# Kernel optimization log

Measured on AMD Instinct MI355X. Metric: run time of the kernel, lower is better.

## Reference

```python
import jax, jax.numpy as jnp
import numpy as np

D_H = 768
HEAD = 12
D_ATTN = D_H // HEAD


def setup_inputs() -> dict:
    key = jax.random.key(0)
    ks = jax.random.split(key, 9)
    bz, slen = 2, 4096
    scale = 1.0 / np.sqrt(D_H)
    return {
        "v": jax.random.normal(ks[0], (bz, slen, D_H), jnp.float32),
        "k": jax.random.normal(ks[1], (bz, slen, D_H), jnp.float32),
        "q": jax.random.normal(ks[2], (bz, slen, D_H), jnp.float32),
        "mask": jax.random.randint(ks[3], (bz, 1, 1, slen), 0, 2, jnp.int32),
        "w_v": jax.random.normal(ks[4], (D_H, D_H), jnp.float32) * scale,
        "w_k": jax.random.normal(ks[5], (D_H, D_H), jnp.float32) * scale,
        "w_q": jax.random.normal(ks[6], (D_H, D_H), jnp.float32) * scale,
        "w_o": jax.random.normal(ks[7], (D_H, D_H), jnp.float32) * scale,
        "b_o": jax.random.normal(ks[8], (D_H,), jnp.float32) * 0.02,
    }


def _split_head(x, seq_len):
    # (bz, len, d_h) -> (bz, head, len, d_attn)
    bz = x.shape[0]
    return x.reshape(bz, seq_len, HEAD, D_ATTN).transpose(0, 2, 1, 3)


def reference(v, k, q, mask, w_v, w_k, w_q, w_o, b_o):
    len_k, len_q = k.shape[1], q.shape[1]
    vh = _split_head(v @ w_v, len_k)   # (bz, head, len_k, d_attn)
    kh = _split_head(k @ w_k, len_k)
    qh = _split_head(q @ w_q, len_q)
    # scaled dot-product attention with additive mask
    weight = jnp.einsum("bhqd,bhkd->bhqk", qh, kh) / jnp.sqrt(
        jnp.asarray(D_ATTN, jnp.float32)
    )
    weight = weight + mask.astype(weight.dtype) * (-1e9)
    scale_weight = jax.nn.softmax(weight, axis=-1)
    attn = jnp.einsum("bhqk,bhkd->bhqd", scale_weight, vh)
    attn = attn.transpose(0, 2, 1, 3).reshape(-1, len_q, D_H)
    return attn @ w_o + b_o
```

## Files before the change

kernel.cpp:

```cpp
#include <hip/hip_runtime.h>
#include <hip/hip_bf16.h>

#define SLEN 4096
#define DH 768
#define NHEAD 12
#define DA 64

using short8 = __attribute__((ext_vector_type(8))) short;
using f32x4  = __attribute__((ext_vector_type(4))) float;
typedef unsigned uv2 __attribute__((ext_vector_type(2)));

static __device__ __forceinline__ unsigned short f2b(float f) {
    union { __hip_bfloat16 h; unsigned short u; } c;
    c.h = __float2bfloat16(f);
    return c.u;
}

static __device__ __forceinline__ unsigned pkbf(float a, float b) {
    __hip_bfloat162 h = __float22bfloat162_rn(float2{a, b});
    union { __hip_bfloat162 h; unsigned u; } c; c.h = h; return c.u;
}

static __device__ __forceinline__ float fexp2(float x) {
    float r; asm("v_exp_f32 %0, %1" : "=v"(r) : "v"(x)); return r;
}

static __device__ __forceinline__ void swap32(unsigned& a, unsigned& b, int g1) {
#if __has_builtin(__builtin_amdgcn_permlane32_swap)
    uv2 r = __builtin_amdgcn_permlane32_swap(a, b, false, false);
    a = r.x; b = r.y;
#else
    unsigned own = g1 ? b : a, send = g1 ? a : b;
    unsigned recv = __shfl_xor(send, 32);
    unsigned nlo = g1 ? recv : own;
    unsigned nhi = g1 ? own : recv;
    a = nlo; b = nhi;
#endif
}

static __device__ __forceinline__ void swap16(unsigned& a, unsigned& b, int g0) {
#if __has_builtin(__builtin_amdgcn_permlane16_swap)
    uv2 r = __builtin_amdgcn_permlane16_swap(a, b, false, false);
    a = r.x; b = r.y;
#else
    unsigned own = g0 ? b : a, send = g0 ? a : b;
    unsigned recv = __shfl_xor(send, 16);
    unsigned nlo = g0 ? recv : own;
    unsigned nhi = g0 ? own : recv;
    a = nlo; b = nhi;
#endif
}

#define GLD_LDS16(gp, lp) __builtin_amdgcn_global_load_lds( \
    (const __attribute__((address_space(1))) unsigned int*)(gp), \
    (__attribute__((address_space(3))) unsigned int*)(lp), 16, 0, 0)

#define CSCALE 0.18033688011f
#define BIASSTRIDE 4352

__global__ __launch_bounds__(256) void wtrans4(const float* __restrict__ w_v, const float* __restrict__ w_k,
                                               const float* __restrict__ w_q, const float* __restrict__ w_o,
                                               unsigned short* __restrict__ WtV, unsigned short* __restrict__ WtK,
                                               unsigned short* __restrict__ WtQ, unsigned short* __restrict__ WtO,
                                               const int* __restrict__ mask, int* __restrict__ idx,
                                               float* __restrict__ biasC, int* __restrict__ nktArr) {
    const int z = blockIdx.y;
    const int t = threadIdx.x;
    if (z == 4) {
        if (blockIdx.x >= 2) return;
        __shared__ int psum[256];
        const int b = blockIdx.x;
        const int s0 = t * 16;
        const int* mb = mask + b * SLEN;
        int keep[16]; int cnt = 0;
#pragma unroll
        for (int j = 0; j < 16; ++j) { keep[j] = (mb[s0 + j] == 0); cnt += keep[j]; }
        psum[t] = cnt;
        __syncthreads();
        for (int off = 1; off < 256; off <<= 1) {
            int v = psum[t];
            int u = (t >= off) ? psum[t - off] : 0;
            __syncthreads();
            psum[t] = v + u;
            __syncthreads();
        }
        int excl = psum[t] - cnt;
        int total = psum[255];
        int* ib = idx + b * SLEN;
#pragma unroll
        for (int j = 0; j < 16; ++j)
            if (keep[j]) ib[excl++] = s0 + j;
        for (int j = total + t; j < SLEN; j += 256) ib[j] = 0;
        int nkt = (total + 63) >> 6;
        if (nkt < 2) nkt = 2;
        if (t == 0) nktArr[b] = nkt;
        float* bb = biasC + b * BIASSTRIDE;
        for (int j = t; j < BIASSTRIDE; j += 256) bb[j] = (j < total) ? 0.f : -1.442695041e9f;
        return;
    }
    const float* W = (z == 0) ? w_v : (z == 1) ? w_k : (z == 2) ? w_q : w_o;
    unsigned short* Wt = (z == 0) ? WtV : (z == 1) ? WtK : (z == 2) ? WtQ : WtO;
    __shared__ float tile[64][65];
    const int tk = blockIdx.x / 12, tn = blockIdx.x % 12;
    const int k0 = tk * 64, n0 = tn * 64;
#pragma unroll
    for (int i = 0; i < 4; ++i) {
        int uid = t + 256 * i;
        int r = uid >> 4, c = (uid & 15) * 4;
        float4 v4 = *reinterpret_cast<const float4*>(W + (size_t)(k0 + r) * DH + n0 + c);
        tile[r][c] = v4.x; tile[r][c + 1] = v4.y; tile[r][c + 2] = v4.z; tile[r][c + 3] = v4.w;
    }
    __syncthreads();
#pragma unroll
    for (int i = 0; i < 2; ++i) {
        int uid = t + 256 * i;
        int n = uid >> 3, c = (uid & 7) * 8;
        union { unsigned short us[8]; uint4 u; } pk;
#pragma unroll
        for (int j = 0; j < 8; ++j) pk.us[j] = f2b(tile[c + j][n]);
        *reinterpret_cast<uint4*>(Wt + (size_t)(n0 + n) * DH + k0 + c) = pk.u;
    }
}

__global__ __launch_bounds__(256, 3) void proj3(const float* __restrict__ vin, const float* __restrict__ kin,
                                                const float* __restrict__ qin,
                                                const unsigned short* __restrict__ WtV,
                                                const unsigned short* __restrict__ WtK,
                                                const unsigned short* __restrict__ WtQ,
                                                unsigned short* __restrict__ Vh,
                                                unsigned short* __restrict__ Kh,
                                                unsigned short* __restrict__ Qh) {
    __shared__ __align__(16) char smem[49152];
    const int t = threadIdx.x;
    const int w = t >> 6, lane = t & 63, lr = lane & 15, lg = lane >> 4;
    const int zz = blockIdx.y;
    const int z = zz / 6, panel = zz % 6;
    const float* X = (z == 0) ? vin : (z == 1) ? kin : qin;
    const unsigned short* Wt = (z == 0) ? WtV : (z == 1) ? WtK : WtQ;
    const int row0 = blockIdx.x * 128;
    const int n0 = panel * 128;

    const float* ap[4];
#pragma unroll
    for (int g = 0; g < 4; ++g) {
        int row = w * 32 + g * 8 + (lane >> 3);
        int cj = (lane & 7) ^ (row & 7);
        ap[g] = X + (size_t)(row0 + row) * DH + cj * 4;
    }
    const unsigned short* bp2[2];
#pragma unroll
    for (int g = 0; g < 2; ++g) {
        int n = w * 32 + g * 16 + (lane >> 2);
        int cj = (lane & 3) ^ (n & 3);
        bp2[g] = Wt + (size_t)(n0 + n) * DH + cj * 8;
    }

    const int arow = w * 32 + lr;
    const int lr7 = lr & 7, lr3 = lr & 3;

    f32x4 acc[2][8] = {};

#define STAGE(PAR) do {                                                              \
        char* ab_ = smem + (PAR) * 16384 + w * 4096;                                 \
        char* bb_ = smem + 32768 + (PAR) * 8192 + w * 2048;                          \
        GLD_LDS16(ap[0], ab_);         GLD_LDS16(ap[1], ab_ + 1024);                 \
        GLD_LDS16(ap[2], ab_ + 2048);  GLD_LDS16(ap[3], ab_ + 3072);                 \
        GLD_LDS16(bp2[0], bb_);        GLD_LDS16(bp2[1], bb_ + 1024);                \
        ap[0] += 32; ap[1] += 32; ap[2] += 32; ap[3] += 32;                          \
        bp2[0] += 32; bp2[1] += 32;                                                  \
    } while (0)

    STAGE(0);
    __syncthreads();

    for (int kt = 0; kt < 24; ++kt) {
        const int par = kt & 1;
        if (kt < 23) STAGE(par ^ 1);
        const char* bufA = smem + par * 16384;
        const char* bufB = smem + 32768 + par * 8192;
        short8 af[2];
#pragma unroll
        for (int mi = 0; mi < 2; ++mi) {
            int r = arow + mi * 16;
            f32x4 alo = *reinterpret_cast<const f32x4*>(bufA + r * 128 + ((2 * lg) ^ lr7) * 16);
            f32x4 ahi = *reinterpret_cast<const f32x4*>(bufA + r * 128 + ((2 * lg + 1) ^ lr7) * 16);
            union { unsigned u[4]; short8 s; } pk;
            pk.u[0] = pkbf(alo[0], alo[1]);
            pk.u[1] = pkbf(alo[2], alo[3]);
            pk.u[2] = pkbf(ahi[0], ahi[1]);
            pk.u[3] = pkbf(ahi[2], ahi[3]);
            af[mi] = pk.s;
        }
        __builtin_amdgcn_s_setprio(1);
#pragma unroll
        for (int ni = 0; ni < 8; ++ni) {
            int n = ni * 16 + lr;
            short8 bf = *reinterpret_cast<const short8*>(bufB + n * 64 + (lg ^ lr3) * 16);
            acc[0][ni] = __builtin_amdgcn_mfma_f32_16x16x32_bf16(af[0], bf, acc[0][ni], 0, 0, 0);
            acc[1][ni] = __builtin_amdgcn_mfma_f32_16x16x32_bf16(af[1], bf, acc[1][ni], 0, 0, 0);
        }
        __builtin_amdgcn_s_setprio(0);
        __syncthreads();
    }
#undef STAGE

    const int b = row0 >> 12, s0 = row0 & 4095;
    unsigned short* Y = (z == 0) ? Vh : (z == 1) ? Kh : Qh;
    const float scale = (z == 2) ? CSCALE : 1.0f;
#pragma unroll
    for (int mi = 0; mi < 2; ++mi)
#pragma unroll
        for (int ni = 0; ni < 8; ++ni) {
            int n = n0 + ni * 16 + lr;
            int h = n >> 6, d = n & 63;
#pragma unroll
            for (int r = 0; r < 4; ++r) {
                int s = s0 + w * 32 + mi * 16 + lg * 4 + r;
                Y[(size_t)((b * NHEAD + h) * SLEN + s) * DA + d] = f2b(acc[mi][ni][r] * scale);
            }
        }
}

__global__ __launch_bounds__(256) void kvcompact(const unsigned short* __restrict__ Kh,
                                                 const unsigned short* __restrict__ Vh,
                                                 unsigned short* __restrict__ Khc,
                                                 unsigned short* __restrict__ VhTc,
                                                 const int* __restrict__ idx,
                                                 const int* __restrict__ nktArr) {
    const int jt = blockIdx.x;
    const int bh = blockIdx.y;
    const int b = bh / NHEAD;
    if (jt >= nktArr[b]) return;
    const int j0 = jt * 64;
    __shared__ unsigned short tile[64][72];
    const int t = threadIdx.x;
    const int r = t >> 2, c = t & 3;
    const int src = idx[b * SLEN + j0 + r];
    const size_t kin  = ((size_t)bh * SLEN + src) * DA + c * 16;
    const size_t kout = ((size_t)bh * SLEN + j0 + r) * DA + c * 16;
    uint4 kv0 = *reinterpret_cast<const uint4*>(Kh + kin);
    uint4 kv1 = *reinterpret_cast<const uint4*>(Kh + kin + 8);
    *reinterpret_cast<uint4*>(Khc + kout) = kv0;
    *reinterpret_cast<uint4*>(Khc + kout + 8) = kv1;
    uint4 vv0 = *reinterpret_cast<const uint4*>(Vh + kin);
    uint4 vv1 = *reinterpret_cast<const uint4*>(Vh + kin + 8);
    *reinterpret_cast<uint4*>(&tile[r][c * 16]) = vv0;
    *reinterpret_cast<uint4*>(&tile[r][c * 16 + 8]) = vv1;
    __syncthreads();
    const int d = t & 63, jc = (t >> 6) * 16;
    union { unsigned short us[8]; uint4 u; } p0, p1;
#pragma unroll
    for (int j = 0; j < 8; ++j) { p0.us[j] = tile[jc + j][d]; p1.us[j] = tile[jc + 8 + j][d]; }
    unsigned short* dst = VhTc + ((size_t)bh * DA + d) * SLEN + j0 + jc;
    *reinterpret_cast<uint4*>(dst) = p0.u;
    *reinterpret_cast<uint4*>(dst + 8) = p1.u;
}

__global__ __launch_bounds__(256, 3) void attn_kernel(const unsigned short* __restrict__ Qh,
                                                      const unsigned short* __restrict__ Kh,
                                                      const unsigned short* __restrict__ VhT,
                                                      const float* __restrict__ biasC,
                                                      const int* __restrict__ nktArr,
                                                      unsigned short* __restrict__ AT) {
    __shared__ __align__(16) char smem[49152];
    const int t = threadIdx.x;
    const int w = t >> 6, lane = t & 63, lr = lane & 15, lg = lane >> 4;
    const int g0 = (lane >> 4) & 1, g1 = (lane >> 5) & 1;
    const int lr7 = lr & 7;

    const int i = blockIdx.x;
    const int bh = (i & 7) * 3 + ((i >> 3) >> 5);
    const int qb = (i >> 3) & 31;
    const int b = bh / NHEAD;
    const int q0 = qb * 128;
    const size_t base = (size_t)bh * SLEN * DA;
    const int wq0 = q0 + w * 32;
    const int nkt = nktArr[b];

    short8 qf[2][2];
#pragma unroll
    for (int mi = 0; mi < 2; ++mi)
#pragma unroll
        for (int ks = 0; ks < 2; ++ks)
            qf[mi][ks] = *reinterpret_cast<const short8*>(
                Qh + base + (size_t)(wq0 + mi * 16 + lr) * DA + ks * 32 + lg * 8);

    const int uid0 = (w << 6) | lane;
    const int r0 = uid0 >> 3;
    const int sc0 = ((uid0 & 7) ^ (r0 & 7)) * 8;
    const unsigned short* kp = Kh + base + (size_t)r0 * DA + sc0;
    const unsigned short* vp = VhT + ((size_t)bh * DA + r0) * SLEN + sc0;
    const float* bp = biasC + b * BIASSTRIDE + lg * 4;

    const int a0 = lr * 128 + ((lg) ^ lr7) * 16;
    const int a1 = lr * 128 + ((4 + lg) ^ lr7) * 16;

    f32x4 st[2][4];
    f32x4 oacc[2][4] = {};
    f32x4 oacc_l[2] = {};
    f32x4 bias_c[4];
    short8 pa[2][2];
    union { unsigned u[4]; short8 s; } ones;
    ones.u[0] = 0x3F803F80u; ones.u[1] = 0x3F803F80u; ones.u[2] = 0x3F803F80u; ones.u[3] = 0x3F803F80u;

#define STAGE(CB) do {                                                   \
        GLD_LDS16(kp,              smem + (CB) + w * 1024);              \
        GLD_LDS16(kp + 2048,       smem + (CB) + (4 + w) * 1024);        \
        GLD_LDS16(vp,              smem + (CB) + 8192 + w * 1024);       \
        GLD_LDS16(vp + 32 * SLEN,  smem + (CB) + 8192 + (4 + w) * 1024); \
        kp += 64 * DA; vp += 64;                                         \
    } while (0)

#define BIASLD do {                                                              \
        _Pragma("unroll") for (int ni = 0; ni < 4; ++ni)                         \
            bias_c[ni] = *reinterpret_cast<const f32x4*>(bp + ni * 16);          \
        bp += 64;                                                                \
    } while (0)

#define QKT(NB) do {                                                                           \
        _Pragma("unroll") for (int ni = 0; ni < 4; ++ni) {                                     \
            short8 kf0 = *reinterpret_cast<const short8*>(smem + (NB) + ni * 2048 + a0);       \
            short8 kf1 = *reinterpret_cast<const short8*>(smem + (NB) + ni * 2048 + a1);       \
            st[0][ni] = __builtin_amdgcn_mfma_f32_16x16x32_bf16(kf1, qf[0][1],                 \
                        __builtin_amdgcn_mfma_f32_16x16x32_bf16(kf0, qf[0][0], bias_c[ni], 0, 0, 0), 0, 0, 0); \
            st[1][ni] = __builtin_amdgcn_mfma_f32_16x16x32_bf16(kf1, qf[1][1],                 \
                        __builtin_amdgcn_mfma_f32_16x16x32_bf16(kf0, qf[1][0], bias_c[ni], 0, 0, 0), 0, 0, 0); \
        }                                                                                      \
    } while (0)

#define PV(CB) do {                                                                                  \
        _Pragma("unroll") for (int ni = 0; ni < 4; ++ni) {                                           \
            short8 vf0 = *reinterpret_cast<const short8*>(smem + (CB) + 8192 + ni * 2048 + a0);      \
            short8 vf1 = *reinterpret_cast<const short8*>(smem + (CB) + 8192 + ni * 2048 + a1);      \
            oacc[0][ni] = __builtin_amdgcn_mfma_f32_16x16x32_bf16(vf0, pa[0][0], oacc[0][ni], 0, 0, 0); \
            oacc[0][ni] = __builtin_amdgcn_mfma_f32_16x16x32_bf16(vf1, pa[0][1], oacc[0][ni], 0, 0, 0); \
            oacc[1][ni] = __builtin_amdgcn_mfma_f32_16x16x32_bf16(vf0, pa[1][0], oacc[1][ni], 0, 0, 0); \
            oacc[1][ni] = __builtin_amdgcn_mfma_f32_16x16x32_bf16(vf1, pa[1][1], oacc[1][ni], 0, 0, 0); \
        }                                                                                            \
        oacc_l[0] = __builtin_amdgcn_mfma_f32_16x16x32_bf16(ones.s, pa[0][0], oacc_l[0], 0, 0, 0);   \
        oacc_l[0] = __builtin_amdgcn_mfma_f32_16x16x32_bf16(ones.s, pa[0][1], oacc_l[0], 0, 0, 0);   \
        oacc_l[1] = __builtin_amdgcn_mfma_f32_16x16x32_bf16(ones.s, pa[1][0], oacc_l[1], 0, 0, 0);   \
        oacc_l[1] = __builtin_amdgcn_mfma_f32_16x16x32_bf16(ones.s, pa[1][1], oacc_l[1], 0, 0, 0);   \
    } while (0)

#define SOFTMAX do {                                                                               \
        _Pragma("unroll") for (int mi = 0; mi < 2; ++mi) {                                         \
            unsigned D[8];                                                                         \
            _Pragma("unroll") for (int ni = 0; ni < 4; ++ni) {                                     \
                float p0 = fexp2(st[mi][ni][0]);                                                   \
                float p1 = fexp2(st[mi][ni][1]);                                                   \
                float p2 = fexp2(st[mi][ni][2]);                                                   \
                float p3 = fexp2(st[mi][ni][3]);                                                   \
                D[ni * 2] = pkbf(p0, p1);                                                          \
                D[ni * 2 + 1] = pkbf(p2, p3);                                                      \
            }                                                                                      \
            swap32(D[0], D[2], g1); swap32(D[1], D[3], g1);                                        \
            swap32(D[4], D[6], g1); swap32(D[5], D[7], g1);                                        \
            swap16(D[0], D[2], g0); swap16(D[1], D[3], g0);                                        \
            swap16(D[4], D[6], g0); swap16(D[5], D[7], g0);                                        \
            union { unsigned u[4]; short8 s; } c0, c1;                                             \
            c0.u[0] = D[0]; c0.u[1] = D[1]; c0.u[2] = D[2]; c0.u[3] = D[3];                        \
            c1.u[0] = D[4]; c1.u[1] = D[5]; c1.u[2] = D[6]; c1.u[3] = D[7];                        \
            pa[mi][0] = c0.s; pa[mi][1] = c1.s;                                                    \
        }                                                                                          \
    } while (0)

    STAGE(0);
    __syncthreads();
    STAGE(16384);
    BIASLD;
    __builtin_amdgcn_s_setprio(1);
    QKT(0);
    __builtin_amdgcn_s_setprio(0);

    int cb = 0, nb = 16384, nnb = 32768;
    for (int kt = 0; kt < nkt - 1; ++kt) {
        SOFTMAX;
        __syncthreads();
        if (kt < nkt - 2) STAGE(nnb);
        BIASLD;
        __builtin_amdgcn_s_setprio(1);
        QKT(nb);
        PV(cb);
        __builtin_amdgcn_s_setprio(0);
        int tmp = cb; cb = nb; nb = nnb; nnb = tmp;
    }
    SOFTMAX;
    __builtin_amdgcn_s_setprio(1);
    PV(cb);
    __builtin_amdgcn_s_setprio(0);

#undef SOFTMAX
#undef PV
#undef QKT
#undef BIASLD
#undef STAGE

    {
        __syncthreads();
        float inv[2];
        inv[0] = 1.0f / oacc_l[0][0];
        inv[1] = 1.0f / oacc_l[1][0];
        unsigned* Obw = reinterpret_cast<unsigned*>(smem) + w * (32 * 36);
#pragma unroll
        for (int mi = 0; mi < 2; ++mi)
#pragma unroll
            for (int ni = 0; ni < 4; ++ni) {
                uint2 pr;
                pr.x = pkbf(oacc[mi][ni][0] * inv[mi], oacc[mi][ni][1] * inv[mi]);
                pr.y = pkbf(oacc[mi][ni][2] * inv[mi], oacc[mi][ni][3] * inv[mi]);
                *reinterpret_cast<uint2*>(&Obw[(mi * 16 + lr) * 36 + ni * 8 + lg * 2]) = pr;
            }
        __syncthreads();
        int row = lane >> 1, half = lane & 1;
        int qg = q0 + w * 32 + row;
        unsigned short* dst = AT + (size_t)(b * SLEN + qg) * DH + (bh % NHEAD) * DA + half * 32;
#pragma unroll
        for (int c = 0; c < 4; ++c) {
            uint4 v = *reinterpret_cast<const uint4*>(&Obw[row * 36 + half * 16 + c * 4]);
            *reinterpret_cast<uint4*>(dst + c * 8) = v;
        }
    }
}

__global__ __launch_bounds__(256) void proj_out(const unsigned short* __restrict__ X,
                                                const unsigned short* __restrict__ Wt,
                                                const float* __restrict__ bias,
                                                float* __restrict__ Y) {
    __shared__ unsigned short As[128][40];
    __shared__ unsigned short Bs[64][40];
    const int t = threadIdx.x;
    const int w = t >> 6, lane = t & 63, lr = lane & 15, lg = lane >> 4;
    const int row0 = blockIdx.x * 128;
    const int n0 = blockIdx.y * 64;
    f32x4 acc[2][4] = {};
    for (int kt = 0; kt < 24; ++kt) {
        const int k0 = kt * 32;
#pragma unroll
        for (int i = 0; i < 2; ++i) {
            int uid = t + 256 * i;
            int r = uid >> 2, c = (uid & 3) * 8;
            *reinterpret_cast<uint4*>(&As[r][c]) =
                *reinterpret_cast<const uint4*>(X + (size_t)(row0 + r) * DH + k0 + c);
        }
        {
            int n = t >> 2, c = (t & 3) * 8;
            *reinterpret_cast<uint4*>(&Bs[n][c]) =
                *reinterpret_cast<const uint4*>(Wt + (size_t)(n0 + n) * DH + k0 + c);
        }
        __syncthreads();
        short8 af[2], bf[4];
#pragma unroll
        for (int mi = 0; mi < 2; ++mi)
            af[mi] = *reinterpret_cast<const short8*>(&As[w * 32 + mi * 16 + lr][lg * 8]);
#pragma unroll
        for (int ni = 0; ni < 4; ++ni)
            bf[ni] = *reinterpret_cast<const short8*>(&Bs[ni * 16 + lr][lg * 8]);
#pragma unroll
        for (int mi = 0; mi < 2; ++mi)
#pragma unroll
            for (int ni = 0; ni < 4; ++ni)
                acc[mi][ni] = __builtin_amdgcn_mfma_f32_16x16x32_bf16(af[mi], bf[ni], acc[mi][ni], 0, 0, 0);
        __syncthreads();
    }
#pragma unroll
    for (int ni = 0; ni < 4; ++ni) {
        float bv = bias[n0 + ni * 16 + lr];
#pragma unroll
        for (int mi = 0; mi < 2; ++mi)
#pragma unroll
            for (int r = 0; r < 4; ++r) {
                int row = row0 + w * 32 + mi * 16 + lg * 4 + r;
                Y[(size_t)row * DH + n0 + ni * 16 + lr] = acc[mi][ni][r] + bv;
            }
    }
}

extern "C" void kernel_launch(void* const* d_in, const int* in_sizes, int n_in,
                              void* d_out, int out_size, void* d_ws, size_t ws_size,
                              hipStream_t stream) {
    const float* v   = (const float*)d_in[0];
    const float* k   = (const float*)d_in[1];
    const float* q   = (const float*)d_in[2];
    const int*  mask = (const int*)d_in[3];
    const float* w_v = (const float*)d_in[4];
    const float* w_k = (const float*)d_in[5];
    const float* w_q = (const float*)d_in[6];
    const float* w_o = (const float*)d_in[7];
    const float* b_o = (const float*)d_in[8];
    float* out = (float*)d_out;

    char* ws = (char*)d_ws;
    unsigned short* Qh  = (unsigned short*)(ws);
    unsigned short* KhD = (unsigned short*)(ws + 12582912);
    unsigned short* VhD = (unsigned short*)(ws + 25165824);
    unsigned short* Khc = (unsigned short*)(ws + 37748736);
    unsigned short* VhTc= (unsigned short*)(ws + 50331648);
    unsigned short* AT  = KhD;
    unsigned short* WtV = (unsigned short*)(ws + 62914560);
    unsigned short* WtK = WtV + 589824;
    unsigned short* WtQ = WtK + 589824;
    unsigned short* WtO = WtQ + 589824;
    float* biasC = (float*)(ws + 67633152);
    int*   idxA  = (int*)(ws + 67667968);
    int*   nktA  = (int*)(ws + 67700736);

    wtrans4<<<dim3(144, 5), 256, 0, stream>>>(w_v, w_k, w_q, w_o, WtV, WtK, WtQ, WtO,
                                              mask, idxA, biasC, nktA);
    proj3<<<dim3(64, 18), 256, 0, stream>>>(v, k, q, WtV, WtK, WtQ, VhD, KhD, Qh);
    kvcompact<<<dim3(64, 24), 256, 0, stream>>>(KhD, VhD, Khc, VhTc, idxA, nktA);
    attn_kernel<<<768, 256, 0, stream>>>(Qh, Khc, VhTc, biasC, nktA, AT);
    proj_out<<<dim3(64, 12), 256, 0, stream>>>(AT, WtO, b_o, out);
}
```

Before: 154.8 us.

## Double-buffer proj_out with async global-to-LDS loads and XOR-swizzled tiles

Result: faster. 147.0 us (-5.0%).

```diff
diff --git a/kernel.cpp b/kernel.cpp
--- a/kernel.cpp
+++ b/kernel.cpp
@@ -357,6 +357,29 @@
             swap32(D[0], D[2], g1); swap32(D[1], D[3], g1);                                        \
             swap32(D[4], D[6], g1); swap32(D[5], D[7], g1);                                        \
             swap16(D[0], D[2], g0); swap16(D[1], D[3], g0);                                        \
+            swap16(D[4], D[6], g0); swap16(D[4 - 4], D[2], g0);                                    \
+            union { unsigned u[4]; short8 s; } c0, c1;                                             \
+            c0.u[0] = D[0]; c0.u[1] = D[1]; c0.u[2] = D[2]; c0.u[3] = D[3];                        \
+            c1.u[0] = D[4]; c1.u[1] = D[5]; c1.u[2] = D[6]; c1.u[3] = D[7];                        \
+            pa[mi][0] = c0.s; pa[mi][1] = c1.s;                                                    \
+        }                                                                                          \
+    } while (0)
+
+#undef SOFTMAX
+#define SOFTMAX do {                                                                               \
+        _Pragma("unroll") for (int mi = 0; mi < 2; ++mi) {                                         \
+            unsigned D[8];                                                                         \
+            _Pragma("unroll") for (int ni = 0; ni < 4; ++ni) {                                     \
+                float p0 = fexp2(st[mi][ni][0]);                                                   \
+                float p1 = fexp2(st[mi][ni][1]);                                                   \
+                float p2 = fexp2(st[mi][ni][2]);                                                   \
+                float p3 = fexp2(st[mi][ni][3]);                                                   \
+                D[ni * 2] = pkbf(p0, p1);                                                          \
+                D[ni * 2 + 1] = pkbf(p2, p3);                                                      \
+            }                                                                                      \
+            swap32(D[0], D[2], g1); swap32(D[1], D[3], g1);                                        \
+            swap32(D[4], D[6], g1); swap32(D[5], D[7], g1);                                        \
+            swap16(D[0], D[2], g0); swap16(D[1], D[3], g0);                                        \
             swap16(D[4], D[6], g0); swap16(D[5], D[7], g0);                                        \
             union { unsigned u[4]; short8 s; } c0, c1;                                             \
             c0.u[0] = D[0]; c0.u[1] = D[1]; c0.u[2] = D[2]; c0.u[3] = D[3];                        \
@@ -423,46 +446,80 @@
     }
 }
 
-__global__ __launch_bounds__(256) void proj_out(const unsigned short* __restrict__ X,
-                                                const unsigned short* __restrict__ Wt,
-                                                const float* __restrict__ bias,
-                                                float* __restrict__ Y) {
-    __shared__ unsigned short As[128][40];
-    __shared__ unsigned short Bs[64][40];
+__global__ __launch_bounds__(256, 3) void proj_out(const unsigned short* __restrict__ X,
+                                                   const unsigned short* __restrict__ Wt,
+                                                   const float* __restrict__ bias,
+                                                   float* __restrict__ Y) {
+    __shared__ __align__(16) char smem[49152];
     const int t = threadIdx.x;
     const int w = t >> 6, lane = t & 63, lr = lane & 15, lg = lane >> 4;
     const int row0 = blockIdx.x * 128;
     const int n0 = blockIdx.y * 64;
+    const int lr7 = lr & 7;
+
+    const unsigned short* ap[4];
+#pragma unroll
+    for (int g = 0; g < 4; ++g) {
+        int row = w * 32 + g * 8 + (lane >> 3);
+        int cj = (lane & 7) ^ (row & 7);
+        ap[g] = X + (size_t)(row0 + row) * DH + cj * 8;
+    }
+    const unsigned short* bp2[2];
+#pragma unroll
+    for (int g = 0; g < 2; ++g) {
+        int n = w * 16 + g * 8 + (lane >> 3);
+        int cj = (lane & 7) ^ (n & 7);
+        bp2[g] = Wt + (size_t)(n0 + n) * DH + cj * 8;
+    }
+
     f32x4 acc[2][4] = {};
-    for (int kt = 0; kt < 24; ++kt) {
-        const int k0 = kt * 32;
-#pragma unroll
-        for (int i = 0; i < 2; ++i) {
-            int uid = t + 256 * i;
-            int r = uid >> 2, c = (uid & 3) * 8;
-            *reinterpret_cast<uint4*>(&As[r][c]) =
-                *reinterpret_cast<const uint4*>(X + (size_t)(row0 + r) * DH + k0 + c);
-        }
-        {
-            int n = t >> 2, c = (t & 3) * 8;
-            *reinterpret_cast<uint4*>(&Bs[n][c]) =
-                *reinterpret_cast<const uint4*>(Wt + (size_t)(n0 + n) * DH + k0 + c);
-        }
+
+#define STAGE_O(PAR) do {                                                            \
+        char* ab_ = smem + (PAR) * 16384 + w * 4096;                                 \
+        char* bb_ = smem + 32768 + (PAR) * 8192 + w * 2048;                          \
+        GLD_LDS16(ap[0], ab_);         GLD_LDS16(ap[1], ab_ + 1024);                 \
+        GLD_LDS16(ap[2], ab_ + 2048);  GLD_LDS16(ap[3], ab_ + 3072);                 \
+        GLD_LDS16(bp2[0], bb_);        GLD_LDS16(bp2[1], bb_ + 1024);                \
+        ap[0] += 64; ap[1] += 64; ap[2] += 64; ap[3] += 64;                          \
+        bp2[0] += 64; bp2[1] += 64;                                                  \
+    } while (0)
+
+    STAGE_O(0);
+    __syncthreads();
+
+    for (int kt = 0; kt < 12; ++kt) {
+        const int par = kt & 1;
+        if (kt < 11) STAGE_O(par ^ 1);
+        const char* bufA = smem + par * 16384;
+        const char* bufB = smem + 32768 + par * 8192;
+        short8 af[2][2], bf[4][2];
+#pragma unroll
+        for (int mi = 0; mi < 2; ++mi) {
+            int r = w * 32 + mi * 16 + lr;
+#pragma unroll
+            for (int ks = 0; ks < 2; ++ks)
+                af[mi][ks] = *reinterpret_cast<const short8*>(bufA + r * 128 + ((ks * 4 + lg) ^ lr7) * 16);
+        }
+#pragma unroll
+        for (int ni = 0; ni < 4; ++ni) {
+            int n = ni * 16 + lr;
+#pragma unroll
+            for (int ks = 0; ks < 2; ++ks)
+                bf[ni][ks] = *reinterpret_cast<const short8*>(bufB + n * 128 + ((ks * 4 + lg) ^ lr7) * 16);
+        }
+        __builtin_amdgcn_s_setprio(1);
+#pragma unroll
+        for (int mi = 0; mi < 2; ++mi)
+#pragma unroll
+            for (int ni = 0; ni < 4; ++ni) {
+                acc[mi][ni] = __builtin_amdgcn_mfma_f32_16x16x32_bf16(af[mi][0], bf[ni][0], acc[mi][ni], 0, 0, 0);
+                acc[mi][ni] = __builtin_amdgcn_mfma_f32_16x16x32_bf16(af[mi][1], bf[ni][1], acc[mi][ni], 0, 0, 0);
+            }
+        __builtin_amdgcn_s_setprio(0);
         __syncthreads();
-        short8 af[2], bf[4];
-#pragma unroll
-        for (int mi = 0; mi < 2; ++mi)
-            af[mi] = *reinterpret_cast<const short8*>(&As[w * 32 + mi * 16 + lr][lg * 8]);
-#pragma unroll
-        for (int ni = 0; ni < 4; ++ni)
-            bf[ni] = *reinterpret_cast<const short8*>(&Bs[ni * 16 + lr][lg * 8]);
-#pragma unroll
-        for (int mi = 0; mi < 2; ++mi)
-#pragma unroll
-            for (int ni = 0; ni < 4; ++ni)
-                acc[mi][ni] = __builtin_amdgcn_mfma_f32_16x16x32_bf16(af[mi], bf[ni], acc[mi][ni], 0, 0, 0);
-        __syncthreads();
-    }
+    }
+#undef STAGE_O
+
 #pragma unroll
     for (int ni = 0; ni < 4; ++ni) {
         float bv = bias[n0 + ni * 16 + lr];
```
